# Performance work log

Measured on AMD Instinct MI355X. Metric: run time of the kernel, lower is better.

Reference implementation:

```python
import jax, jax.numpy as jnp
import numpy as np

N = 20000   # nodes per graph
E = 320000  # edges per graph
D_IN, D_H = 128, 304


def _param(key, shape, fan_in):
    return jax.random.normal(key, shape, dtype=jnp.float32) / np.sqrt(fan_in)


def setup_inputs() -> dict:
    key = jax.random.key(0)
    ks = jax.random.split(key, 20)
    inp = {}
    for i, name in enumerate(['x1', 'x2', 'x3']):
        inp[name] = jax.random.normal(ks[i], (N, D_IN), dtype=jnp.float32)
    for i, name in enumerate(['src1', 'dst1', 'src2', 'dst2', 'src3', 'dst3']):
        inp[name] = jax.random.randint(ks[3 + i], (E,), 0, N, dtype=jnp.int32)
    # shared GraphConv weights (DGL GraphConv: h = norm_agg(x) @ W + b)
    inp['W1'] = _param(ks[9], (D_IN, D_H), D_IN)
    inp['b1'] = jnp.zeros((D_H,), jnp.float32)
    inp['W2'] = _param(ks[10], (D_H, D_H), D_H)
    inp['b2'] = jnp.zeros((D_H,), jnp.float32)
    inp['W3'] = _param(ks[11], (D_H, D_H), D_H)
    inp['b3'] = jnp.zeros((D_H,), jnp.float32)
    # MLP head: 304 -> 128 -> 64 -> 1
    inp['fW1'] = _param(ks[12], (D_H, 128), D_H)
    inp['fb1'] = jnp.zeros((128,), jnp.float32)
    inp['fW2'] = _param(ks[13], (128, 64), 128)
    inp['fb2'] = jnp.zeros((64,), jnp.float32)
    inp['fW3'] = _param(ks[14], (64, 1), 64)
    inp['fb3'] = jnp.zeros((1,), jnp.float32)
    return inp


def gcn_conv(x, src, dst, W, b):
    # DGL GraphConv, norm='both': h = D_in^{-1/2} A D_out^{-1/2} x W + b
    ones = jnp.ones((src.shape[0],), x.dtype)
    out_deg = jnp.clip(jax.ops.segment_sum(ones, src, num_segments=N), 1.0)
    in_deg = jnp.clip(jax.ops.segment_sum(ones, dst, num_segments=N), 1.0)
    h = x * jax.lax.rsqrt(out_deg)[:, None]
    agg = jax.ops.segment_sum(h[src], dst, num_segments=N)  # [N, d] SpMM
    agg = agg * jax.lax.rsqrt(in_deg)[:, None]
    return agg @ W + b


def reference(x1, x2, x3, src1, dst1, src2, dst2, src3, dst3,
              W1, b1, W2, b2, W3, b3, fW1, fb1, fW2, fb2, fW3, fb3):
    def branch(x, src, dst):
        x = jax.nn.relu(gcn_conv(x, src, dst, W1, b1))
        x = jax.nn.relu(gcn_conv(x, src, dst, W2, b2))
        x = jax.nn.relu(gcn_conv(x, src, dst, W3, b3))
        return x

    h1 = branch(x1, src1, dst1)
    h2 = branch(x2, src2, dst2)
    h3 = branch(x3, src3, dst3)
    # multi_graph_opt='max': max over all nodes of all three graphs -> [304]
    pooled = jnp.max(jnp.concatenate([h1, h2, h3], axis=0), axis=0)
    # output_opt='fc': MLP head with sigmoid
    z = jax.nn.relu(pooled @ fW1 + fb1)
    z = jax.nn.relu(z @ fW2 + fb2)
    return jax.nn.sigmoid(z @ fW3 + fb3)  # shape [1]
```

## Files before the change

### kernel.cpp

```cpp
#include <hip/hip_runtime.h>
#include <hip/hip_bf16.h>
#include <math.h>

#define NODES 20000
#define EDGES 320000
#define NB 3
#define TOTN (NODES * NB)
#define TOTE (EDGES * NB)
#define D_IN 128
#define D_H 304
#define SCAN_B 59
#define SLICES 40
#define SLICE_E (EDGES / SLICES)
#define ZX TOTN
#define ZQ (TOTN + 96)
#define PACKB 7500

typedef __attribute__((ext_vector_type(4))) float f32x4;
typedef __attribute__((ext_vector_type(2))) float f32x2;

__device__ __forceinline__ void gload16(const void* g, void* l) {
    __builtin_amdgcn_global_load_lds(
        (const __attribute__((address_space(1))) unsigned*)g,
        (__attribute__((address_space(3))) unsigned*)l, 16, 0, 0);
}

__global__ void k_pack_prepw(const float4* __restrict__ x1, const float4* __restrict__ x2,
                             const float4* __restrict__ x3, const float* __restrict__ inv_out,
                             unsigned* __restrict__ q,
                             const float* __restrict__ W1, const float* __restrict__ W2,
                             const float* __restrict__ W3,
                             unsigned char* __restrict__ Wt1, unsigned char* __restrict__ Wt2,
                             unsigned char* __restrict__ Wt3) {
    if (blockIdx.x < PACKB) {
        const int per = NODES * D_IN / 4;
        int i = blockIdx.x * 256 + threadIdx.x;
        const float4* s; int j;
        if (i < per)          { s = x1; j = i; }
        else if (i < 2 * per) { s = x2; j = i - per; }
        else                  { s = x3; j = i - 2 * per; }
        float4 v = s[j];
        float sc = inv_out[i >> 5];
        int p = __builtin_amdgcn_cvt_pk_fp8_f32(v.x * sc, v.y * sc, 0, false);
        p = __builtin_amdgcn_cvt_pk_fp8_f32(v.z * sc, v.w * sc, p, true);
        q[i] = (unsigned)p;
    } else {
        const int N1 = D_H * 128, N2 = D_H * 320;
        int id = (blockIdx.x - PACKB) * 256 + threadIdx.x;
        const float* W; unsigned char* Wt; int K, Kpad, lid;
        if (id < N1)                { W = W1; Wt = Wt1; K = 128; Kpad = 128; lid = id; }
        else if (id < N1 + N2)      { W = W2; Wt = Wt2; K = 304; Kpad = 320; lid = id - N1; }
        else if (id < N1 + 2 * N2)  { W = W3; Wt = Wt3; K = 304; Kpad = 320; lid = id - N1 - N2; }
        else return;
        int n = lid / Kpad, k = lid - n * Kpad;
        unsigned char v = 0;
        if (k < K) {
            float w = W[k * D_H + n];
            v = (unsigned char)(__builtin_amdgcn_cvt_pk_fp8_f32(w, w, 0, false) & 0xff);
        }
        Wt[lid] = v;
    }
}

__global__ __launch_bounds__(256, 1) void k_hist(
    const int* __restrict__ s1, const int* __restrict__ d1,
    const int* __restrict__ s2, const int* __restrict__ d2,
    const int* __restrict__ s3, const int* __restrict__ d3,
    unsigned short* __restrict__ partial_in, unsigned short* __restrict__ partial_out,
    int* __restrict__ gctr) {
    __shared__ int hist[NODES];
    if (blockIdx.x == 0 && blockIdx.y == 0 && threadIdx.x == 0) *gctr = 0;
    int g = blockIdx.x / SLICES, s = blockIdx.x % SLICES;
    bool isOut = (blockIdx.y == 1);
    const int* ep;
    if (isOut) ep = (g == 0) ? s1 : ((g == 1) ? s2 : s3);
    else       ep = (g == 0) ? d1 : ((g == 1) ? d2 : d3);
    ep += s * SLICE_E;
    for (int i = threadIdx.x; i < NODES; i += 256) hist[i] = 0;
    __syncthreads();
    const int4* ep4 = (const int4*)ep;
    for (int i = threadIdx.x; i < SLICE_E / 4; i += 256) {
        int4 v = ep4[i];
        atomicAdd(&hist[v.x], 1);
        atomicAdd(&hist[v.y], 1);
        atomicAdd(&hist[v.z], 1);
        atomicAdd(&hist[v.w], 1);
    }
    __syncthreads();
    unsigned short* po = (isOut ? partial_out : partial_in) + (size_t)blockIdx.x * NODES;
    for (int i = threadIdx.x; i < NODES; i += 256) po[i] = (unsigned short)hist[i];
}

__global__ void k_degscan(const unsigned short* __restrict__ partial_in,
                          const unsigned short* __restrict__ partial_out,
                          float* __restrict__ inv_in, float* __restrict__ inv_out,
                          int* __restrict__ row_ptr, int* __restrict__ rend,
                          int* __restrict__ gctr) {
    __shared__ int wsum[16];
    __shared__ int sbase;
    int b = blockIdx.x, t = threadIdx.x;
    int i = b * 1024 + t;
    int lane = t & 63, wid = t >> 6;
    int v = 0;
    if (i < TOTN) {
        int g = i / NODES, ln = i - g * NODES;
        const unsigned short* pi = partial_in + (size_t)g * SLICES * NODES + ln;
        const unsigned short* po = partial_out + (size_t)g * SLICES * NODES + ln;
        int ci = 0, co = 0;
        #pragma unroll
        for (int s = 0; s < SLICES; s++) { ci += pi[s * NODES]; co += po[s * NODES]; }
        v = ci;
        inv_in[i]  = 1.0f / sqrtf((float)max(ci, 1));
        inv_out[i] = 1.0f / sqrtf((float)max(co, 1));
    }
    int sv = v;
    #pragma unroll
    for (int o = 1; o < 64; o <<= 1) {
        int u = __shfl_up(sv, o, 64);
        if (lane >= o) sv += u;
    }
    if (lane == 63) wsum[wid] = sv;
    __syncthreads();
    if (t < 16) {
        int w = wsum[t];
        #pragma unroll
        for (int o = 1; o < 16; o <<= 1) {
            int u = __shfl_up(w, o, 16);
            if (t >= o) w += u;
        }
        wsum[t] = w;
    }
    __syncthreads();
    if (t == 0) sbase = atomicAdd(gctr, wsum[15]);
    __syncthreads();
    int wbase = (wid > 0) ? wsum[wid - 1] : 0;
    if (i < TOTN) {
        int rp = sbase + wbase + sv - v;
        row_ptr[i] = rp;
        rend[i] = rp + v;
    }
}

__global__ void k_offC(const int* __restrict__ row_ptr,
                       const unsigned short* __restrict__ partial_in,
                       int* __restrict__ O,
                       int* __restrict__ csr_slack, unsigned* __restrict__ x8z,
                       unsigned* __restrict__ q8z, int* __restrict__ pooled) {
    int n = blockIdx.x * 256 + threadIdx.x;
    if (n >= TOTN) {
        int ex = n - TOTN;
        if (ex < 32) csr_slack[ex] = 0;
        else if (ex < 64) x8z[ex - 32] = 0;
        else if (ex < 144) q8z[ex - 64] = 0;
        else if (ex < 464) pooled[ex - 144] = 0;
        return;
    }
    int rp = row_ptr[n];
    int g = n / NODES, ln = n - g * NODES;
    const unsigned short* pi = partial_in + (size_t)g * SLICES * NODES + ln;
    int* on = O + (size_t)g * SLICES * NODES + ln;
    int run = rp;
    #pragma unroll
    for (int s = 0; s < SLICES; s++) {
        on[s * NODES] = run;
        run += pi[s * NODES];
    }
}

__global__ __launch_bounds__(256, 1) void k_fill2(
    const int* __restrict__ s1, const int* __restrict__ d1,
    const int* __restrict__ s2, const int* __restrict__ d2,
    const int* __restrict__ s3, const int* __restrict__ d3,
    const int* __restrict__ O, int* __restrict__ csr) {
    __shared__ int cur[NODES];
    int g = blockIdx.x / SLICES, s = blockIdx.x % SLICES;
    const int* sp = (g == 0) ? s1 : ((g == 1) ? s2 : s3);
    const int* dp = (g == 0) ? d1 : ((g == 1) ? d2 : d3);
    sp += s * SLICE_E; dp += s * SLICE_E;
    const int* on = O + (size_t)blockIdx.x * NODES;
    for (int i = threadIdx.x; i < NODES; i += 256) cur[i] = on[i];
    __syncthreads();
    int base = g * NODES;
    const int4* sp4 = (const int4*)sp;
    const int4* dp4 = (const int4*)dp;
    for (int i = threadIdx.x; i < SLICE_E / 4; i += 256) {
        int4 dv = dp4[i];
        int4 sv = sp4[i];
        int p0 = atomicAdd(&cur[dv.x], 1); csr[p0] = sv.x + base;
        int p1 = atomicAdd(&cur[dv.y], 1); csr[p1] = sv.y + base;
        int p2 = atomicAdd(&cur[dv.z], 1); csr[p2] = sv.z + base;
        int p3 = atomicAdd(&cur[dv.w], 1); csr[p3] = sv.w + base;
    }
}

__global__ void k_spmm_l1(const uint2* __restrict__ h, unsigned char* __restrict__ agg,
                          const int* __restrict__ row_ptr, const int* __restrict__ rend,
                          const int* __restrict__ csr,
                          const float* __restrict__ inv_in) {
    int n = blockIdx.x * 4 + (threadIdx.x >> 6);
    int lane = threadIdx.x & 63;
    int s = lane >> 4;
    int off = lane & 15;
    f32x2 a[4];
    #pragma unroll
    for (int j = 0; j < 4; j++) a[j] = (f32x2){0.f, 0.f};
    int k0 = row_ptr[n], k1 = rend[n];
    int deg = k1 - k0;
    const int* cp = csr + k0 + s;
    int e[8];
    #pragma unroll
    for (int j = 0; j < 8; j++) {
        int ev = cp[4 * j];
        e[j] = (s + 4 * j < deg) ? ev : ZX;
    }
    uint2 u[8];
    #pragma unroll
    for (int j = 0; j < 8; j++)
        if (4 * j < deg) u[j] = h[(size_t)e[j] * 16 + off];
    #pragma unroll
    for (int j = 0; j < 8; j++) {
        if (4 * j < deg) {
            a[0] += __builtin_amdgcn_cvt_pk_f32_fp8(u[j].x, false);
            a[1] += __builtin_amdgcn_cvt_pk_f32_fp8(u[j].x, true);
            a[2] += __builtin_amdgcn_cvt_pk_f32_fp8(u[j].y, false);
            a[3] += __builtin_amdgcn_cvt_pk_f32_fp8(u[j].y, true);
        }
    }
    for (int k = k0 + 32 + s; k < k1; k += 4) {
        int e0 = csr[k];
        uint2 u0 = h[(size_t)e0 * 16 + off];
        a[0] += __builtin_amdgcn_cvt_pk_f32_fp8(u0.x, false);
        a[1] += __builtin_amdgcn_cvt_pk_f32_fp8(u0.x, true);
        a[2] += __builtin_amdgcn_cvt_pk_f32_fp8(u0.y, false);
        a[3] += __builtin_amdgcn_cvt_pk_f32_fp8(u0.y, true);
    }
    float r[8];
    #pragma unroll
    for (int j = 0; j < 4; j++) {
        #pragma unroll
        for (int c = 0; c < 2; c++) {
            float v = a[j][c];
            r[2 * j + c] = v + __shfl(v, lane + 16, 64)
                             + __shfl(v, lane + 32, 64)
                             + __shfl(v, lane + 48, 64);
        }
    }
    if (lane < 16) {
        float wi = inv_in[n];
        int d0 = __builtin_amdgcn_cvt_pk_fp8_f32(r[0] * wi, r[1] * wi, 0, false);
        d0 = __builtin_amdgcn_cvt_pk_fp8_f32(r[2] * wi, r[3] * wi, d0, true);
        int d1 = __builtin_amdgcn_cvt_pk_fp8_f32(r[4] * wi, r[5] * wi, 0, false);
        d1 = __builtin_amdgcn_cvt_pk_fp8_f32(r[6] * wi, r[7] * wi, d1, true);
        uint2 st; st.x = (unsigned)d0; st.y = (unsigned)d1;
        *(uint2*)(agg + (size_t)n * 128 + lane * 8) = st;
    }
}

__global__ void k_spmm_big(const uint4* __restrict__ h, unsigned char* __restrict__ agg,
                           const int* __restrict__ row_ptr, const int* __restrict__ rend,
                           const int* __restrict__ csr,
                           const float* __restrict__ inv_in) {
    int n = blockIdx.x * 4 + (threadIdx.x >> 6);
    int lane = threadIdx.x & 63;
    int s = lane / 20;
    int off = lane % 20;
    f32x2 a[8];
    #pragma unroll
    for (int j = 0; j < 8; j++) a[j] = (f32x2){0.f, 0.f};
    int k0 = row_ptr[n], k1 = rend[n];
    int deg = k1 - k0;
    int degg = (s < 3) ? deg : 0;
    const int* cp = csr + k0 + s;
    int e[8];
    #pragma unroll
    for (int j = 0; j < 8; j++) {
        int ev = cp[3 * j];
        e[j] = (s + 3 * j < degg) ? ev : ZQ;
    }
    uint4 u[8];
    #pragma unroll
    for (int j = 0; j < 8; j++)
        if (3 * j < deg) u[j] = h[(size_t)e[j] * 20 + off];
    #pragma unroll
    for (int j = 0; j < 8; j++) {
        if (3 * j < deg) {
            a[0] += __builtin_amdgcn_cvt_pk_f32_fp8(u[j].x, false);
            a[1] += __builtin_amdgcn_cvt_pk_f32_fp8(u[j].x, true);
            a[2] += __builtin_amdgcn_cvt_pk_f32_fp8(u[j].y, false);
            a[3] += __builtin_amdgcn_cvt_pk_f32_fp8(u[j].y, true);
            a[4] += __builtin_amdgcn_cvt_pk_f32_fp8(u[j].z, false);
            a[5] += __builtin_amdgcn_cvt_pk_f32_fp8(u[j].z, true);
            a[6] += __builtin_amdgcn_cvt_pk_f32_fp8(u[j].w, false);
            a[7] += __builtin_amdgcn_cvt_pk_f32_fp8(u[j].w, true);
        }
    }
    int k1g = k0 + degg;
    for (int k = k0 + 24 + s; k < k1g; k += 3) {
        int e0 = csr[k];
        uint4 u0 = h[(size_t)e0 * 20 + off];
        a[0] += __builtin_amdgcn_cvt_pk_f32_fp8(u0.x, false);
        a[1] += __builtin_amdgcn_cvt_pk_f32_fp8(u0.x, true);
        a[2] += __builtin_amdgcn_cvt_pk_f32_fp8(u0.y, false);
        a[3] += __builtin_amdgcn_cvt_pk_f32_fp8(u0.y, true);
        a[4] += __builtin_amdgcn_cvt_pk_f32_fp8(u0.z, false);
        a[5] += __builtin_amdgcn_cvt_pk_f32_fp8(u0.z, true);
        a[6] += __builtin_amdgcn_cvt_pk_f32_fp8(u0.w, false);
        a[7] += __builtin_amdgcn_cvt_pk_f32_fp8(u0.w, true);
    }
    float r[16];
    #pragma unroll
    for (int j = 0; j < 8; j++) {
        #pragma unroll
        for (int c = 0; c < 2; c++) {
            float v = a[j][c];
            r[2 * j + c] = v + __shfl(v, lane + 20, 64) + __shfl(v, lane + 40, 64);
        }
    }
    if (lane < 20) {
        float wi = inv_in[n];
        int d0 = __builtin_amdgcn_cvt_pk_fp8_f32(r[0] * wi, r[1] * wi, 0, false);
        d0 = __builtin_amdgcn_cvt_pk_fp8_f32(r[2] * wi, r[3] * wi, d0, true);
        int d1 = __builtin_amdgcn_cvt_pk_fp8_f32(r[4] * wi, r[5] * wi, 0, false);
        d1 = __builtin_amdgcn_cvt_pk_fp8_f32(r[6] * wi, r[7] * wi, d1, true);
        int d2 = __builtin_amdgcn_cvt_pk_fp8_f32(r[8] * wi, r[9] * wi, 0, false);
        d2 = __builtin_amdgcn_cvt_pk_fp8_f32(r[10] * wi, r[11] * wi, d2, true);
        int d3 = __builtin_amdgcn_cvt_pk_fp8_f32(r[12] * wi, r[13] * wi, 0, false);
        d3 = __builtin_amdgcn_cvt_pk_fp8_f32(r[14] * wi, r[15] * wi, d3, true);
        uint4 st; st.x = (unsigned)d0; st.y = (unsigned)d1; st.z = (unsigned)d2; st.w = (unsigned)d3;
        *(uint4*)(agg + (size_t)n * 320 + lane * 16) = st;
    }
}

template <int MODE>
__global__ __launch_bounds__(256, 2) void k_gemm_mfma(
    const unsigned char* __restrict__ A, int lda,
    const unsigned char* __restrict__ Wt,
    const float* __restrict__ bias,
    const float* __restrict__ inv_out,
    unsigned char* __restrict__ C8, int* __restrict__ gpool, int M, int K) {
    __shared__ char SM[40960];
    __shared__ int pmax[D_H];
    char* As = SM;
    char* Bs = SM + 8192;
    int tid = threadIdx.x;
    int wv = tid >> 6, lane = tid & 63;
    int quad = lane >> 4, lrow = lane & 15;
    int bm = blockIdx.x * 128;

    if (MODE == 1) {
        for (int i = tid; i < D_H; i += 256) pmax[i] = 0;
    }

    f32x4 acc[2][19];
    #pragma unroll
    for (int r = 0; r < 2; r++)
        #pragma unroll
        for (int t = 0; t < 19; t++) acc[r][t] = (f32x4){0.f, 0.f, 0.f, 0.f};

    int swz = (lrow & 3) ^ (lrow >> 2);
    int hb = (quad & 1) * 8;

    for (int kt = 0; kt < K; kt += 64) {
        #pragma unroll
        for (int j = 0; j < 2; j++) {
            int c = j * 256 + tid;
            int row = c >> 2, xc = c & 3;
            int col = xc ^ (row & 3) ^ ((row >> 2) & 3);
            gload16(A + (size_t)(bm + row) * lda + kt + col * 16, As + c * 16);
        }
        #pragma unroll
        for (int j = 0; j < 5; j++) {
            int c = j * 256 + tid;
            if (c < 1216) {
                int row = c >> 2, xc = c & 3;
                int col = xc ^ (row & 3) ^ ((row >> 2) & 3);
                gload16(Wt + (size_t)row * K + kt + col * 16, Bs + c * 16);
            }
        }
        __syncthreads();
        #pragma unroll
        for (int sub = 0; sub < 2; sub++) {
            int c0 = sub * 2 + (quad >> 1);
            int cx = (c0 ^ swz) * 16 + hb;
            int ra = wv * 32 + lrow;
            long long a0 = *(const long long*)(As + ra * 64 + cx);
            long long a1 = *(const long long*)(As + (ra + 16) * 64 + cx);
            #pragma unroll
            for (int t = 0; t < 19; t++) {
                long long b = *(const long long*)(Bs + (t * 16 + lrow) * 64 + cx);
                acc[0][t] = __builtin_amdgcn_mfma_f32_16x16x32_fp8_fp8(a0, b, acc[0][t], 0, 0, 0);
                acc[1][t] = __builtin_amdgcn_mfma_f32_16x16x32_fp8_fp8(a1, b, acc[1][t], 0, 0, 0);
            }
        }
        __syncthreads();
    }
    if (MODE == 0) {
        unsigned char* OUT = (unsigned char*)SM;
        if (tid < 128) *(uint4*)(OUT + tid * 320 + 304) = make_uint4(0u, 0u, 0u, 0u);
        #pragma unroll
        for (int t = 0; t < 19; t++) {
            int col = t * 16 + lrow;
            float bv = bias[col];
            #pragma unroll
            for (int r = 0; r < 2; r++) {
                int rl = wv * 32 + r * 16 + quad * 4;
                #pragma unroll
                for (int g = 0; g < 4; g++) {
                    int row = bm + rl + g;
                    float sc = inv_out[min(row, M - 1)];
                    float v = fmaxf(acc[r][t][g] + bv, 0.f) * sc;
                    int p = __builtin_amdgcn_cvt_pk_fp8_f32(v, v, 0, false);
                    OUT[(rl + g) * 320 + col] = (unsigned char)(p & 0xff);
                }
            }
        }
        __syncthreads();
        #pragma unroll
        for (int j = 0; j < 10; j++) {
            int c = j * 256 + tid;
            *(uint4*)(C8 + (size_t)bm * 320 + (size_t)c * 16) = *(const uint4*)(OUT + c * 16);
        }
    } else {
        #pragma unroll
        for (int t = 0; t < 19; t++) {
            int col = t * 16 + lrow;
            float bv = bias[col];
            float m = 0.f;
            #pragma unroll
            for (int r = 0; r < 2; r++) {
                int rbase = bm + wv * 32 + r * 16 + quad * 4;
                #pragma unroll
                for (int g = 0; g < 4; g++) {
                    int row = rbase + g;
                    if (row < M) m = fmaxf(m, fmaxf(acc[r][t][g] + bv, 0.f));
                }
            }
            atomicMax(&pmax[col], __float_as_int(m));
        }
        __syncthreads();
        for (int i = tid; i < D_H; i += 256)
            atomicMax(&gpool[i], pmax[i]);
    }
}

__global__ void k_mlp(const int* __restrict__ pooled_i,
                      const float* __restrict__ fW1, const float* __restrict__ fb1,
                      const float* __restrict__ fW2, const float* __restrict__ fb2,
                      const float* __restrict__ fW3, const float* __restrict__ fb3,
                      float* __restrict__ out) {
    __shared__ float p[D_H];
    __shared__ float z1[128];
    __shared__ float z2[64];
    int t = threadIdx.x;
    if (t < D_H) p[t] = __int_as_float(pooled_i[t]);
    __syncthreads();
    if (t < 128) {
        float acc = fb1[t];
        for (int k = 0; k < D_H; k++) acc += p[k] * fW1[k * 128 + t];
        z1[t] = fmaxf(acc, 0.f);
    }
    __syncthreads();
    if (t < 64) {
        float acc = fb2[t];
        for (int k = 0; k < 128; k++) acc += z1[k] * fW2[k * 64 + t];
        z2[t] = fmaxf(acc, 0.f);
    }
    __syncthreads();
    if (t == 0) {
        float acc = fb3[0];
        for (int k = 0; k < 64; k++) acc += z2[k] * fW3[k];
        out[0] = 1.f / (1.f + expf(-acc));
    }
}

extern "C" void kernel_launch(void* const* d_in, const int* in_sizes, int n_in,
                              void* d_out, int out_size, void* d_ws, size_t ws_size,
                              hipStream_t stream) {
    const float* x1 = (const float*)d_in[0];
    const float* x2 = (const float*)d_in[1];
    const float* x3 = (const float*)d_in[2];
    const int* src1 = (const int*)d_in[3];
    const int* dst1 = (const int*)d_in[4];
    const int* src2 = (const int*)d_in[5];
    const int* dst2 = (const int*)d_in[6];
    const int* src3 = (const int*)d_in[7];
    const int* dst3 = (const int*)d_in[8];
    const float* W1 = (const float*)d_in[9];
    const float* b1 = (const float*)d_in[10];
    const float* W2 = (const float*)d_in[11];
    const float* b2 = (const float*)d_in[12];
    const float* W3 = (const float*)d_in[13];
    const float* b3 = (const float*)d_in[14];
    const float* fW1 = (const float*)d_in[15];
    const float* fb1 = (const float*)d_in[16];
    const float* fW2 = (const float*)d_in[17];
    const float* fb2 = (const float*)d_in[18];
    const float* fW3 = (const float*)d_in[19];
    const float* fb3 = (const float*)d_in[20];
    float* out = (float*)d_out;

    char* w = (char*)d_ws;
    unsigned* X8       = (unsigned*)w;      w += (size_t)(TOTN + 1) * 32 * 4;
    unsigned char* Q8  = (unsigned char*)w; w += (size_t)(TOTN + 128) * 320;
    unsigned char* P8  = (unsigned char*)w; w += (size_t)(TOTN + 128) * 320;
    unsigned char* Wt1 = (unsigned char*)w; w += (size_t)D_H * 128;
    unsigned char* Wt2 = (unsigned char*)w; w += (size_t)D_H * 320;
    unsigned char* Wt3 = (unsigned char*)w; w += (size_t)D_H * 320;
    w = (char*)(((size_t)w + 255) & ~(size_t)255);
    unsigned short* partial_in  = (unsigned short*)w; w += (size_t)NB * SLICES * NODES * 2;
    unsigned short* partial_out = (unsigned short*)w; w += (size_t)NB * SLICES * NODES * 2;
    int* O         = (int*)w;    w += (size_t)NB * SLICES * NODES * 4;
    float* inv_out = (float*)w;  w += (size_t)TOTN * 4;
    float* inv_in  = (float*)w;  w += (size_t)TOTN * 4;
    int* row_ptr   = (int*)w;    w += (size_t)TOTN * 4;
    int* rend      = (int*)w;    w += (size_t)TOTN * 4;
    int* csr       = (int*)w;    w += (size_t)(TOTE + 32) * 4;
    int* pooled    = (int*)w;    w += 320 * 4;
    int* gctr      = (int*)w;    w += 64;

    k_hist<<<dim3(NB * SLICES, 2), 256, 0, stream>>>(src1, dst1, src2, dst2, src3, dst3,
                                                     partial_in, partial_out, gctr);
    k_degscan<<<SCAN_B, 1024, 0, stream>>>(partial_in, partial_out,
                                           inv_in, inv_out, row_ptr, rend, gctr);
    k_pack_prepw<<<PACKB + 912, 256, 0, stream>>>(
        (const float4*)x1, (const float4*)x2, (const float4*)x3, inv_out, X8,
        W1, W2, W3, Wt1, Wt2, Wt3);
    k_offC<<<(TOTN + 464 + 255) / 256, 256, 0, stream>>>(
        row_ptr, partial_in, O, csr + TOTE,
        X8 + (size_t)ZX * 32, (unsigned*)(Q8 + (size_t)ZQ * 320), pooled);
    k_fill2<<<NB * SLICES, 256, 0, stream>>>(src1, dst1, src2, dst2, src3, dst3, O, csr);

    int ggrid = (TOTN + 127) / 128;

    k_spmm_l1<<<TOTN / 4, 256, 0, stream>>>((const uint2*)X8, P8, row_ptr, rend, csr, inv_in);
    k_gemm_mfma<0><<<ggrid, 256, 0, stream>>>(P8, 128, Wt1, b1, inv_out,
                                              Q8, nullptr, TOTN, 128);
    k_spmm_big<<<TOTN / 4, 256, 0, stream>>>((const uint4*)Q8, P8, row_ptr, rend, csr, inv_in);
    k_gemm_mfma<0><<<ggrid, 256, 0, stream>>>(P8, 320, Wt2, b2, inv_out,
                                              Q8, nullptr, TOTN, 320);
    k_spmm_big<<<TOTN / 4, 256, 0, stream>>>((const uint4*)Q8, P8, row_ptr, rend, csr, inv_in);
    k_gemm_mfma<1><<<ggrid, 256, 0, stream>>>(P8, 320, Wt3, b3, nullptr,
                                              nullptr, pooled, TOTN, 320);

    k_mlp<<<1, 320, 0, stream>>>(pooled, fW1, fb1, fW2, fb2, fW3, fb3, out);
}
```

Before: 327.2 us.

## Fuse prep kernels, pack 16-bit LDS histograms, double-buffer GEMM K loop

```diff
diff --git a/kernel.cpp b/kernel.cpp
--- a/kernel.cpp
+++ b/kernel.cpp
@@ -14,7 +14,9 @@
 #define SLICE_E (EDGES / SLICES)
 #define ZX TOTN
 #define ZQ (TOTN + 96)
+#define OFFB 237
 #define PACKB 7500
+#define PREPWB 912
 
 typedef __attribute__((ext_vector_type(4))) float f32x4;
 typedef __attribute__((ext_vector_type(2))) float f32x2;
@@ -23,43 +25,6 @@
     __builtin_amdgcn_global_load_lds(
         (const __attribute__((address_space(1))) unsigned*)g,
         (__attribute__((address_space(3))) unsigned*)l, 16, 0, 0);
-}
-
-__global__ void k_pack_prepw(const float4* __restrict__ x1, const float4* __restrict__ x2,
-                             const float4* __restrict__ x3, const float* __restrict__ inv_out,
-                             unsigned* __restrict__ q,
-                             const float* __restrict__ W1, const float* __restrict__ W2,
-                             const float* __restrict__ W3,
-                             unsigned char* __restrict__ Wt1, unsigned char* __restrict__ Wt2,
-                             unsigned char* __restrict__ Wt3) {
-    if (blockIdx.x < PACKB) {
-        const int per = NODES * D_IN / 4;
-        int i = blockIdx.x * 256 + threadIdx.x;
-        const float4* s; int j;
-        if (i < per)          { s = x1; j = i; }
-        else if (i < 2 * per) { s = x2; j = i - per; }
-        else                  { s = x3; j = i - 2 * per; }
-        float4 v = s[j];
-        float sc = inv_out[i >> 5];
-        int p = __builtin_amdgcn_cvt_pk_fp8_f32(v.x * sc, v.y * sc, 0, false);
-        p = __builtin_amdgcn_cvt_pk_fp8_f32(v.z * sc, v.w * sc, p, true);
-        q[i] = (unsigned)p;
-    } else {
-        const int N1 = D_H * 128, N2 = D_H * 320;
-        int id = (blockIdx.x - PACKB) * 256 + threadIdx.x;
-        const float* W; unsigned char* Wt; int K, Kpad, lid;
-        if (id < N1)                { W = W1; Wt = Wt1; K = 128; Kpad = 128; lid = id; }
-        else if (id < N1 + N2)      { W = W2; Wt = Wt2; K = 304; Kpad = 320; lid = id - N1; }
-        else if (id < N1 + 2 * N2)  { W = W3; Wt = Wt3; K = 304; Kpad = 320; lid = id - N1 - N2; }
-        else return;
-        int n = lid / Kpad, k = lid - n * Kpad;
-        unsigned char v = 0;
-        if (k < K) {
-            float w = W[k * D_H + n];
-            v = (unsigned char)(__builtin_amdgcn_cvt_pk_fp8_f32(w, w, 0, false) & 0xff);
-        }
-        Wt[lid] = v;
-    }
 }
 
 __global__ __launch_bounds__(256, 1) void k_hist(
@@ -68,7 +33,7 @@
     const int* __restrict__ s3, const int* __restrict__ d3,
     unsigned short* __restrict__ partial_in, unsigned short* __restrict__ partial_out,
     int* __restrict__ gctr) {
-    __shared__ int hist[NODES];
+    __shared__ unsigned hist[NODES / 2];
     if (blockIdx.x == 0 && blockIdx.y == 0 && threadIdx.x == 0) *gctr = 0;
     int g = blockIdx.x / SLICES, s = blockIdx.x % SLICES;
     bool isOut = (blockIdx.y == 1);
@@ -76,19 +41,19 @@
     if (isOut) ep = (g == 0) ? s1 : ((g == 1) ? s2 : s3);
     else       ep = (g == 0) ? d1 : ((g == 1) ? d2 : d3);
     ep += s * SLICE_E;
-    for (int i = threadIdx.x; i < NODES; i += 256) hist[i] = 0;
+    for (int i = threadIdx.x; i < NODES / 2; i += 256) hist[i] = 0;
     __syncthreads();
     const int4* ep4 = (const int4*)ep;
     for (int i = threadIdx.x; i < SLICE_E / 4; i += 256) {
         int4 v = ep4[i];
-        atomicAdd(&hist[v.x], 1);
-        atomicAdd(&hist[v.y], 1);
-        atomicAdd(&hist[v.z], 1);
-        atomicAdd(&hist[v.w], 1);
-    }
-    __syncthreads();
-    unsigned short* po = (isOut ? partial_out : partial_in) + (size_t)blockIdx.x * NODES;
-    for (int i = threadIdx.x; i < NODES; i += 256) po[i] = (unsigned short)hist[i];
+        atomicAdd(&hist[v.x >> 1], 1u << ((v.x & 1) << 4));
+        atomicAdd(&hist[v.y >> 1], 1u << ((v.y & 1) << 4));
+        atomicAdd(&hist[v.z >> 1], 1u << ((v.z & 1) << 4));
+        atomicAdd(&hist[v.w >> 1], 1u << ((v.w & 1) << 4));
+    }
+    __syncthreads();
+    unsigned* po = (unsigned*)((isOut ? partial_out : partial_in) + (size_t)blockIdx.x * NODES);
+    for (int i = threadIdx.x; i < NODES / 2; i += 256) po[i] = hist[i];
 }
 
 __global__ void k_degscan(const unsigned short* __restrict__ partial_in,
@@ -141,29 +106,64 @@
     }
 }
 
-__global__ void k_offC(const int* __restrict__ row_ptr,
+__global__ void k_prep(const int* __restrict__ row_ptr,
                        const unsigned short* __restrict__ partial_in,
                        int* __restrict__ O,
                        int* __restrict__ csr_slack, unsigned* __restrict__ x8z,
-                       unsigned* __restrict__ q8z, int* __restrict__ pooled) {
-    int n = blockIdx.x * 256 + threadIdx.x;
-    if (n >= TOTN) {
-        int ex = n - TOTN;
-        if (ex < 32) csr_slack[ex] = 0;
-        else if (ex < 64) x8z[ex - 32] = 0;
-        else if (ex < 144) q8z[ex - 64] = 0;
-        else if (ex < 464) pooled[ex - 144] = 0;
-        return;
-    }
-    int rp = row_ptr[n];
-    int g = n / NODES, ln = n - g * NODES;
-    const unsigned short* pi = partial_in + (size_t)g * SLICES * NODES + ln;
-    int* on = O + (size_t)g * SLICES * NODES + ln;
-    int run = rp;
-    #pragma unroll
-    for (int s = 0; s < SLICES; s++) {
-        on[s * NODES] = run;
-        run += pi[s * NODES];
+                       unsigned* __restrict__ q8z, int* __restrict__ pooled,
+                       const float4* __restrict__ x1, const float4* __restrict__ x2,
+                       const float4* __restrict__ x3, const float* __restrict__ inv_out,
+                       unsigned* __restrict__ q,
+                       const float* __restrict__ W1, const float* __restrict__ W2,
+                       const float* __restrict__ W3,
+                       unsigned char* __restrict__ Wt1, unsigned char* __restrict__ Wt2,
+                       unsigned char* __restrict__ Wt3) {
+    if (blockIdx.x < OFFB) {
+        int n = blockIdx.x * 256 + threadIdx.x;
+        if (n >= TOTN) {
+            int ex = n - TOTN;
+            if (ex < 32) csr_slack[ex] = 0;
+            else if (ex < 64) x8z[ex - 32] = 0;
+            else if (ex < 144) q8z[ex - 64] = 0;
+            else if (ex < 464) pooled[ex - 144] = 0;
+            return;
+        }
+        int rp = row_ptr[n];
+        int g = n / NODES, ln = n - g * NODES;
+        const unsigned short* pi = partial_in + (size_t)g * SLICES * NODES + ln;
+        int* on = O + (size_t)g * SLICES * NODES + ln;
+        int run = rp;
+        #pragma unroll
+        for (int s = 0; s < SLICES; s++) {
+            on[s * NODES] = run;
+            run += pi[s * NODES];
+        }
+    } else if (blockIdx.x < OFFB + PACKB) {
+        const int per = NODES * D_IN / 4;
+        int i = (blockIdx.x - OFFB) * 256 + threadIdx.x;
+        const float4* s; int j;
+        if (i < per)          { s = x1; j = i; }
+        else if (i < 2 * per) { s = x2; j = i - per; }
+        else                  { s = x3; j = i - 2 * per; }
+        float4 v = s[j];
+        float sc = inv_out[i >> 5];
+        int p = __builtin_amdgcn_cvt_pk_fp8_f32(v.x * sc, v.y * sc, 0, false);
+        p = __builtin_amdgcn_cvt_pk_fp8_f32(v.z * sc, v.w * sc, p, true);
+        q[i] = (unsigned)p;
+    } else {
+        const int N1 = D_H * 128, N2 = D_H * 320;
+        int id = (blockIdx.x - OFFB - PACKB) * 256 + threadIdx.x;
+        const float* W; unsigned char* Wt; int K, Kpad, lid;
+        if (id < N1)                { W = W1; Wt = Wt1; K = 128; Kpad = 128; lid = id; }
+        else if (id < N1 + N2)      { W = W2; Wt = Wt2; K = 304; Kpad = 320; lid = id - N1; }
+        else                        { W = W3; Wt = Wt3; K = 304; Kpad = 320; lid = id - N1 - N2; }
+        int n = lid / Kpad, k = lid - n * Kpad;
+        unsigned char v = 0;
+        if (k < K) {
+            float w = W[k * D_H + n];
+            v = (unsigned char)(__builtin_amdgcn_cvt_pk_fp8_f32(w, w, 0, false) & 0xff);
+        }
+        Wt[lid] = v;
     }
 }
 
@@ -338,10 +338,8 @@
     const float* __restrict__ bias,
     const float* __restrict__ inv_out,
     unsigned char* __restrict__ C8, int* __restrict__ gpool, int M, int K) {
-    __shared__ char SM[40960];
+    __shared__ char SM[55296];
     __shared__ int pmax[D_H];
-    char* As = SM;
-    char* Bs = SM + 8192;
     int tid = threadIdx.x;
     int wv = tid >> 6, lane = tid & 63;
     int quad = lane >> 4, lrow = lane & 15;
@@ -360,7 +358,9 @@
     int swz = (lrow & 3) ^ (lrow >> 2);
     int hb = (quad & 1) * 8;
 
-    for (int kt = 0; kt < K; kt += 64) {
+    auto stage = [&](int buf, int kt) {
+        char* As = SM + buf * 27648;
+        char* Bs = As + 8192;
         #pragma unroll
         for (int j = 0; j < 2; j++) {
             int c = j * 256 + tid;
@@ -377,7 +377,15 @@
                 gload16(Wt + (size_t)row * K + kt + col * 16, Bs + c * 16);
             }
         }
-        __syncthreads();
+    };
+
+    int nt = K >> 6;
+    stage(0, 0);
+    __syncthreads();
+    for (int t = 0; t < nt; t++) {
+        if (t + 1 < nt) stage((t + 1) & 1, (t + 1) << 6);
+        const char* As = SM + (t & 1) * 27648;
+        const char* Bs = As + 8192;
         #pragma unroll
         for (int sub = 0; sub < 2; sub++) {
             int c0 = sub * 2 + (quad >> 1);
@@ -386,10 +394,10 @@
             long long a0 = *(const long long*)(As + ra * 64 + cx);
             long long a1 = *(const long long*)(As + (ra + 16) * 64 + cx);
             #pragma unroll
-            for (int t = 0; t < 19; t++) {
-                long long b = *(const long long*)(Bs + (t * 16 + lrow) * 64 + cx);
-                acc[0][t] = __builtin_amdgcn_mfma_f32_16x16x32_fp8_fp8(a0, b, acc[0][t], 0, 0, 0);
-                acc[1][t] = __builtin_amdgcn_mfma_f32_16x16x32_fp8_fp8(a1, b, acc[1][t], 0, 0, 0);
+            for (int u = 0; u < 19; u++) {
+                long long b = *(const long long*)(Bs + (u * 16 + lrow) * 64 + cx);
+                acc[0][u] = __builtin_amdgcn_mfma_f32_16x16x32_fp8_fp8(a0, b, acc[0][u], 0, 0, 0);
+                acc[1][u] = __builtin_amdgcn_mfma_f32_16x16x32_fp8_fp8(a1, b, acc[1][u], 0, 0, 0);
             }
         }
         __syncthreads();
@@ -522,12 +530,11 @@
                                                      partial_in, partial_out, gctr);
     k_degscan<<<SCAN_B, 1024, 0, stream>>>(partial_in, partial_out,
                                            inv_in, inv_out, row_ptr, rend, gctr);
-    k_pack_prepw<<<PACKB + 912, 256, 0, stream>>>(
+    k_prep<<<OFFB + PACKB + PREPWB, 256, 0, stream>>>(
+        row_ptr, partial_in, O, csr + TOTE,
+        X8 + (size_t)ZX * 32, (unsigned*)(Q8 + (size_t)ZQ * 320), pooled,
         (const float4*)x1, (const float4*)x2, (const float4*)x3, inv_out, X8,
         W1, W2, W3, Wt1, Wt2, Wt3);
-    k_offC<<<(TOTN + 464 + 255) / 256, 256, 0, stream>>>(
-        row_ptr, partial_in, O, csr + TOTE,
-        X8 + (size_t)ZX * 32, (unsigned*)(Q8 + (size_t)ZQ * 320), pooled);
     k_fill2<<<NB * SLICES, 256, 0, stream>>>(src1, dst1, src2, dst2, src3, dst3, O, csr);
 
     int ggrid = (TOTN + 127) / 128;
```

Result: no change. 322.5 us (-1.4%).
